# Kernel tuning notes

Hardware: AMD Instinct MI355X
Metric: run time of the kernel (lower is better)

The kernel has to match this reference:

```python
import jax, jax.numpy as jnp
import numpy as np

NUM_HEADS = 16
CAPACITY = 512
ROPE_BASE = 10000.0

def _rope_factor(positions, dim):
    # freqs = exp(linspace(0,-1,dim//2) * log(base)), shape (dim//2,)
    freqs = jnp.exp(jnp.linspace(0.0, -1.0, dim // 2) * jnp.log(jnp.float32(ROPE_BASE)))
    angles = positions[..., None] * freqs            # (..., seq, dim//2)
    return jnp.concatenate([jnp.sin(angles), jnp.cos(angles)], axis=-1)  # (..., seq, dim)

def setup_inputs() -> dict:
    key = jax.random.key(0)
    ks = jax.random.split(key, 6)
    B, Sq, Skv, D = 4, 4096, 4096, 1024
    return {
        "query_seq": jax.random.normal(ks[0], (B, Sq, D), jnp.float32),
        "value_seq": jax.random.normal(ks[1], (B, Skv, D), jnp.float32),
        "router_w": jax.random.normal(ks[2], (1, D), jnp.float32) * 0.02,
        "q_w": jax.random.normal(ks[3], (D, D), jnp.float32) * 0.02,
        "kv_w": jax.random.normal(ks[4], (2 * D, D), jnp.float32) * 0.02,
        "out_w": jax.random.normal(ks[5], (D, D), jnp.float32) * 0.02,
    }

def reference(query_seq, value_seq, router_w, q_w, kv_w, out_w):
    B, Sq, D = query_seq.shape
    Skv = value_seq.shape[1]
    H, C = NUM_HEADS, CAPACITY
    d = D // H

    # router + top-k capacity selection over the sequence dim
    rw = jnp.einsum("bsd,od->bs", query_seq, router_w).astype(jnp.float32)  # (B,Sq)
    top_w, top_idx = jax.lax.top_k(rw, C)                                   # (B,C)

    # gather selected queries
    resampled = jnp.take_along_axis(query_seq, top_idx[:, :, None], axis=1)  # (B,C,D)

    q = jnp.einsum("bcd,ed->bce", resampled, q_w)        # (B,C,H*d)
    kv = jnp.einsum("bsd,ed->bse", value_seq, kv_w)      # (B,Skv,2*H*d)
    k, v = jnp.split(kv, 2, axis=-1)

    q = q.reshape(B, C, H, d).transpose(0, 2, 1, 3)      # (B,H,C,d)
    k = k.reshape(B, Skv, H, d).transpose(0, 2, 1, 3)    # (B,H,Skv,d)
    v = v.reshape(B, Skv, H, d).transpose(0, 2, 1, 3)

    # RoPE-style elementwise modulation (faithful to source: x * cat(sin, cos))
    q_pos = top_idx.astype(jnp.float32)[:, None, :]      # (B,1,C)
    q = q * _rope_factor(q_pos, d)                       # (B,H,C,d)
    k_pos = jnp.arange(Skv, dtype=jnp.float32)[None, :]  # (1,Skv)
    k = k * _rope_factor(k_pos, d)[None]                 # broadcast over (B,H)

    # SDPA
    scores = jnp.einsum("bhcd,bhsd->bhcs", q, k) / jnp.sqrt(jnp.float32(d))
    att = jnp.einsum("bhcs,bhsd->bhcd", jax.nn.softmax(scores, axis=-1), v)

    att = att.transpose(0, 2, 1, 3).reshape(B, C, H * d)  # (B,C,D)
    att = jnp.einsum("bce,de->bcd", att, out_w)           # (B,C,D)

    # weighted scatter back to full sequence
    src = att * top_w[:, :, None]
    out = jnp.zeros_like(query_seq).at[jnp.arange(B)[:, None], top_idx].set(src)
    return out
```

## Files before the change

### kernel.cpp

```cpp
#include <hip/hip_runtime.h>
#include <hip/hip_bf16.h>

#define B_  4
#define SQ  4096
#define SKV 4096
#define DM  1024
#define NH  16
#define HD  64
#define CAP 512

#define ASPLIT 4
#define KVPER  (SKV / ASPLIT)
#define AITERS (KVPER / 64)

typedef __attribute__((ext_vector_type(8))) short    short8;
typedef __attribute__((ext_vector_type(8))) __bf16   bf16v8;
typedef __attribute__((ext_vector_type(4))) float    f32x4;
typedef __attribute__((ext_vector_type(4))) unsigned short ushort4v;

static __device__ __forceinline__ unsigned short f2bf(float f) {
    unsigned u = __float_as_uint(f);
    u += 0x7FFFu + ((u >> 16) & 1u);
    return (unsigned short)(u >> 16);
}

static __device__ __forceinline__ f32x4 mfma_bf16(short8 a, short8 b, f32x4 c) {
    return __builtin_amdgcn_mfma_f32_16x16x32_bf16(
        __builtin_bit_cast(bf16v8, a), __builtin_bit_cast(bf16v8, b), c, 0, 0, 0);
}

#define GLD16(gp, lp)                                                              \
    __builtin_amdgcn_global_load_lds(                                              \
        (__attribute__((address_space(1))) void*)(gp),                             \
        (__attribute__((address_space(3))) void*)(lp), 16, 0, 0)

__global__ void __launch_bounds__(256) k_convert(const float* __restrict__ in,
                                                 unsigned short* __restrict__ out) {
    size_t i = (size_t)blockIdx.x * 256 + threadIdx.x;
    float4 f = ((const float4*)in)[i];
    ushort4v o = { f2bf(f.x), f2bf(f.y), f2bf(f.z), f2bf(f.w) };
    ((ushort4v*)out)[i] = o;
}

__global__ void __launch_bounds__(256) k_rope(float* __restrict__ tab) {
    int g = blockIdx.x * 256 + threadIdx.x;
    int pos = g >> 6, i = g & 63, j = i & 31;
    float freq = expf(-(float)j * (logf(10000.0f) / 31.0f));
    float ang  = (float)pos * freq;
    tab[g] = (i < 32) ? sinf(ang) : cosf(ang);
}

__global__ void __launch_bounds__(256) k_router(const float* __restrict__ q,
                                                const float* __restrict__ wv,
                                                float* __restrict__ rw) {
    int row  = blockIdx.x * 4 + (threadIdx.x >> 6);
    int lane = threadIdx.x & 63;
    const float* p  = q  + (size_t)row * DM + lane * 16;
    const float* wp = wv + lane * 16;
    float s = 0.f;
#pragma unroll
    for (int j = 0; j < 4; j++) {
        float4 a = ((const float4*)p)[j];
        float4 b = ((const float4*)wp)[j];
        s += a.x * b.x + a.y * b.y + a.z * b.z + a.w * b.w;
    }
#pragma unroll
    for (int m = 32; m > 0; m >>= 1) s += __shfl_xor(s, m, 64);
    if (lane == 0) rw[row] = s;
}

__global__ void __launch_bounds__(1024) k_topk(const float* __restrict__ rw,
                                               int* __restrict__ sel,
                                               float* __restrict__ selw) {
    __shared__ unsigned long long keys[4096];
    int b = blockIdx.x, t = threadIdx.x;
    for (int i = t; i < 4096; i += 1024) {
        float v = rw[b * 4096 + i];
        unsigned u = __float_as_uint(v);
        u = (u & 0x80000000u) ? ~u : (u | 0x80000000u);
        keys[i] = ((unsigned long long)(~u) << 32) | (unsigned)i;
    }
    __syncthreads();
    for (int k = 2; k <= 4096; k <<= 1)
        for (int j = k >> 1; j > 0; j >>= 1) {
            for (int i = t; i < 4096; i += 1024) {
                int ixj = i ^ j;
                if (ixj > i) {
                    bool up = ((i & k) == 0);
                    unsigned long long a = keys[i], c = keys[ixj];
                    if ((a > c) == up) { keys[i] = c; keys[ixj] = a; }
                }
            }
            __syncthreads();
        }
    for (int i = t; i < 512; i += 1024) {
        unsigned idx = (unsigned)(keys[i] & 0xFFFFFFFFu);
        sel[b * 512 + i]  = (int)idx;
        selw[b * 512 + i] = rw[b * 4096 + idx];
    }
}

__global__ void __launch_bounds__(256) k_gather(const float* __restrict__ q,
                                                const int* __restrict__ sel,
                                                unsigned short* __restrict__ out) {
    int row = blockIdx.x;
    int b = row >> 9;
    int s = sel[row];
    const float4* src = (const float4*)(q + ((size_t)b * SQ + s) * DM);
    ushort4v* dst = (ushort4v*)(out + (size_t)row * DM);
    float4 f = src[threadIdx.x];
    ushort4v o = { f2bf(f.x), f2bf(f.y), f2bf(f.z), f2bf(f.w) };
    dst[threadIdx.x] = o;
}

template <int MODE, int BN>
__global__ void __launch_bounds__(256) k_gemm(
    const unsigned short* __restrict__ A,
    const unsigned short* __restrict__ Bw,
    int M, int N, int K,
    const float* __restrict__ rope_tab,
    const int* __restrict__ sel,
    const float* __restrict__ selw,
    unsigned short* __restrict__ ok,
    unsigned short* __restrict__ ov,
    unsigned short* __restrict__ obf,
    float* __restrict__ of) {
    constexpr int TN = BN / 32;
    __shared__ unsigned short lA[128 * 32];
    __shared__ unsigned short lB[BN * 32];
    const int tid = threadIdx.x;
    const int w = tid >> 6, lane = tid & 63, quad = lane >> 4, l16 = lane & 15;
    const int wr = w >> 1, wc = w & 1;
    const int mBase = blockIdx.y * 128, nBase = blockIdx.x * BN;

    f32x4 acc[4][TN] = {};

    for (int k0 = 0; k0 < K; k0 += 32) {
#pragma unroll
        for (int is = 0; is < 2; is++) {
            int slot = is * 256 + tid;
            int row = slot >> 2, sc = slot & 3;
            int kc = (sc - (row >> 1)) & 3;
            const char* ga = (const char*)A + (((size_t)(mBase + row) * K) + k0 + kc * 8) * 2;
            GLD16(ga, (char*)lA + slot * 16);
        }
#pragma unroll
        for (int is = 0; is < BN / 64; is++) {
            int slot = is * 256 + tid;
            int row = slot >> 2, sc = slot & 3;
            int kc = (sc - (row >> 1)) & 3;
            const char* gb = (const char*)Bw + (((size_t)(nBase + row) * K) + k0 + kc * 8) * 2;
            GLD16(gb, (char*)lB + slot * 16);
        }
        __syncthreads();
        short8 af[4], bfr[TN];
#pragma unroll
        for (int t = 0; t < 4; t++) {
            int r = wr * 64 + t * 16 + l16;
            af[t] = *(const short8*)&lA[r * 32 + (((quad + (r >> 1)) & 3) * 8)];
        }
#pragma unroll
        for (int t = 0; t < TN; t++) {
            int r = wc * (BN / 2) + t * 16 + l16;
            bfr[t] = *(const short8*)&lB[r * 32 + (((quad + (r >> 1)) & 3) * 8)];
        }
#pragma unroll
        for (int tm = 0; tm < 4; tm++)
#pragma unroll
            for (int tn = 0; tn < TN; tn++)
                acc[tm][tn] = mfma_bf16(af[tm], bfr[tn], acc[tm][tn]);
        __syncthreads();
    }

#pragma unroll
    for (int tm = 0; tm < 4; tm++) {
#pragma unroll
        for (int tn = 0; tn < TN; tn++) {
#pragma unroll
            for (int r = 0; r < 4; r++) {
                int m = mBase + wr * 64 + tm * 16 + quad * 4 + r;
                int n = nBase + wc * (BN / 2) + tn * 16 + l16;
                float v = acc[tm][tn][r];
                if constexpr (MODE == 0) {
                    int b = m >> 12, s = m & 4095;
                    if (n < 1024) {
                        int h = n >> 6, i = n & 63;
                        v *= rope_tab[(s << 6) | i];
                        ok[(((size_t)(b * NH + h) * SKV) + s) * HD + i] = f2bf(v);
                    } else {
                        int e = n - 1024, h = e >> 6, i = e & 63;
                        ov[(((size_t)(b * NH + h) * HD) + i) * SKV + s] = f2bf(v);
                    }
                } else if constexpr (MODE == 1) {
                    int b = m >> 9, c = m & 511;
                    int h = n >> 6, i = n & 63;
                    float rp = rope_tab[(sel[m] << 6) | i];
                    obf[(((size_t)(b * NH + h) * CAP) + c) * HD + i] =
                        f2bf(v * rp * 0.18033688011112042f);
                } else {
                    int b = m >> 9;
                    int s = sel[m];
                    of[(((size_t)b * SQ) + s) * DM + n] = v * selw[m];
                }
            }
        }
    }
}

__global__ void __launch_bounds__(256) k_attention(
    const unsigned short* __restrict__ Q,
    const unsigned short* __restrict__ Kg,
    const unsigned short* __restrict__ Vt,
    float* __restrict__ Opart,
    float* __restrict__ Lpart) {
    __shared__ unsigned short lK[64 * 72];
    __shared__ unsigned short lV[64 * 72];
    __shared__ unsigned short lP[4][32 * 72];
    const int bh = blockIdx.y, z = blockIdx.z;
    const int tid = threadIdx.x, w = tid >> 6, lane = tid & 63;
    const int quad = lane >> 4, l16 = lane & 15;
    const int qb = blockIdx.x * 128 + w * 32;
    const int base = z * KVPER;

    short8 qf[2][2];
#pragma unroll
    for (int rt = 0; rt < 2; rt++) {
        const unsigned short* qp = Q + ((size_t)bh * CAP + qb + rt * 16 + l16) * HD + quad * 8;
        qf[rt][0] = *(const short8*)qp;
        qf[rt][1] = *(const short8*)(qp + 32);
    }

    const unsigned short* kb = Kg + (size_t)bh * SKV * HD;
    const unsigned short* vb = Vt + (size_t)bh * HD * SKV;
    const int sr = tid >> 2, sp = tid & 3;

    f32x4 o[2][4] = {};
    f32x4 lsum[2] = {};
    short8 ones = (short8)0x3F80;

    short8 rk0, rk1, rv0, rv1;
    {
        const short8* srck = (const short8*)(kb + (size_t)(base + sr) * HD + sp * 16);
        rk0 = srck[0]; rk1 = srck[1];
        const short8* srcv = (const short8*)(vb + (size_t)sr * SKV + base + sp * 16);
        rv0 = srcv[0]; rv1 = srcv[1];
    }

    unsigned short* lPw = &lP[w][0];

    for (int it = 0; it < AITERS; it++) {
        __syncthreads();
        *(short8*)&lK[sr * 72 + sp * 16]     = rk0;
        *(short8*)&lK[sr * 72 + sp * 16 + 8] = rk1;
        *(short8*)&lV[sr * 72 + sp * 16]     = rv0;
        *(short8*)&lV[sr * 72 + sp * 16 + 8] = rv1;
        if (it + 1 < AITERS) {
            int s0 = base + (it + 1) * 64;
            const short8* srck = (const short8*)(kb + (size_t)(s0 + sr) * HD + sp * 16);
            rk0 = srck[0]; rk1 = srck[1];
            const short8* srcv = (const short8*)(vb + (size_t)sr * SKV + s0 + sp * 16);
            rv0 = srcv[0]; rv1 = srcv[1];
        }
        __syncthreads();

        f32x4 sc[2][4] = {};
#pragma unroll
        for (int tn = 0; tn < 4; tn++) {
            short8 kf0 = *(const short8*)&lK[(tn * 16 + l16) * 72 + quad * 8];
            short8 kf1 = *(const short8*)&lK[(tn * 16 + l16) * 72 + 32 + quad * 8];
#pragma unroll
            for (int rt = 0; rt < 2; rt++) {
                sc[rt][tn] = mfma_bf16(qf[rt][0], kf0, sc[rt][tn]);
                sc[rt][tn] = mfma_bf16(qf[rt][1], kf1, sc[rt][tn]);
            }
        }
#pragma unroll
        for (int rt = 0; rt < 2; rt++)
#pragma unroll
            for (int tn = 0; tn < 4; tn++)
#pragma unroll
                for (int r = 0; r < 4; r++)
                    lPw[(rt * 16 + quad * 4 + r) * 72 + tn * 16 + l16] =
                        f2bf(exp2f(fminf(sc[rt][tn][r], 86.f)));
#pragma unroll
        for (int kc = 0; kc < 2; kc++) {
            short8 pf0 = *(const short8*)&lPw[(l16) * 72 + kc * 32 + quad * 8];
            short8 pf1 = *(const short8*)&lPw[(16 + l16) * 72 + kc * 32 + quad * 8];
            lsum[0] = mfma_bf16(pf0, ones, lsum[0]);
            lsum[1] = mfma_bf16(pf1, ones, lsum[1]);
#pragma unroll
            for (int tn = 0; tn < 4; tn++) {
                short8 vf = *(const short8*)&lV[(tn * 16 + l16) * 72 + kc * 32 + quad * 8];
                o[0][tn] = mfma_bf16(pf0, vf, o[0][tn]);
                o[1][tn] = mfma_bf16(pf1, vf, o[1][tn]);
            }
        }
    }

    float* Ob = Opart + (((size_t)(z * 64 + bh)) * CAP + qb) * HD;
#pragma unroll
    for (int rt = 0; rt < 2; rt++)
#pragma unroll
        for (int tn = 0; tn < 4; tn++)
#pragma unroll
            for (int r = 0; r < 4; r++)
                Ob[(size_t)(rt * 16 + quad * 4 + r) * HD + tn * 16 + l16] = o[rt][tn][r];
    if (l16 == 0) {
#pragma unroll
        for (int rt = 0; rt < 2; rt++)
#pragma unroll
            for (int r = 0; r < 4; r++)
                Lpart[((size_t)(z * 64 + bh)) * CAP + qb + rt * 16 + quad * 4 + r] = lsum[rt][r];
    }
}

__global__ void __launch_bounds__(256) k_combine(
    const float* __restrict__ Opart, const float* __restrict__ Lpart,
    unsigned short* __restrict__ att) {
    int g = blockIdx.x * 256 + threadIdx.x;
    int dall = g & 1023, c = (g >> 10) & 511, b = g >> 19;
    int h = dall >> 6, dd = dall & 63;
    int bh = b * NH + h;
    float os = 0.f, ls = 0.f;
#pragma unroll
    for (int p = 0; p < ASPLIT; p++) {
        os += Opart[(((size_t)(p * 64 + bh)) * CAP + c) * HD + dd];
        ls += Lpart[((size_t)(p * 64 + bh)) * CAP + c];
    }
    att[g] = f2bf(os / ls);
}

extern "C" void kernel_launch(void* const* d_in, const int* in_sizes, int n_in,
                              void* d_out, int out_size, void* d_ws, size_t ws_size,
                              hipStream_t stream) {
    const float* query    = (const float*)d_in[0];
    const float* value    = (const float*)d_in[1];
    const float* router_w = (const float*)d_in[2];
    const float* q_w      = (const float*)d_in[3];
    const float* kv_w     = (const float*)d_in[4];
    const float* out_w    = (const float*)d_in[5];
    float* out = (float*)d_out;

    char* p = (char*)d_ws;
    unsigned short* value_bf = (unsigned short*)p; p += (size_t)B_ * SKV * DM * 2;
    unsigned short* kvw_bf   = (unsigned short*)p; p += (size_t)2 * DM * DM * 2;
    unsigned short* qw_bf    = (unsigned short*)p; p += (size_t)DM * DM * 2;
    unsigned short* ow_bf    = (unsigned short*)p; p += (size_t)DM * DM * 2;
    unsigned short* res_bf   = (unsigned short*)p; p += (size_t)B_ * CAP * DM * 2;
    unsigned short* q_attn   = (unsigned short*)p; p += (size_t)B_ * CAP * DM * 2;
    unsigned short* kbuf     = (unsigned short*)p; p += (size_t)B_ * SKV * DM * 2;
    unsigned short* vbuf     = (unsigned short*)p; p += (size_t)B_ * SKV * DM * 2;
    unsigned short* att_bf   = (unsigned short*)p; p += (size_t)B_ * CAP * DM * 2;
    float* rope_tab = (float*)p; p += (size_t)SKV * HD * 4;
    float* rw       = (float*)p; p += (size_t)B_ * SQ * 4;
    int*   sel      = (int*)p;   p += (size_t)B_ * CAP * 4;
    float* selw     = (float*)p; p += (size_t)B_ * CAP * 4;
    float* Opart = (float*)value_bf;
    float* Lpart = (float*)res_bf;

    hipMemsetAsync(d_out, 0, (size_t)out_size * sizeof(float), stream);

    k_convert<<<B_ * SKV * DM / 1024, 256, 0, stream>>>(value, value_bf);
    k_convert<<<2 * DM * DM / 1024, 256, 0, stream>>>(kv_w, kvw_bf);
    k_convert<<<DM * DM / 1024, 256, 0, stream>>>(q_w, qw_bf);
    k_convert<<<DM * DM / 1024, 256, 0, stream>>>(out_w, ow_bf);
    k_rope<<<SKV * HD / 256, 256, 0, stream>>>(rope_tab);
    k_router<<<B_ * SQ / 4, 256, 0, stream>>>(query, router_w, rw);
    k_topk<<<B_, 1024, 0, stream>>>(rw, sel, selw);
    k_gather<<<B_ * CAP, 256, 0, stream>>>(query, sel, res_bf);

    k_gemm<0, 128><<<dim3(2 * DM / 128, B_ * SKV / 128), 256, 0, stream>>>(
        value_bf, kvw_bf, B_ * SKV, 2 * DM, DM, rope_tab, nullptr, nullptr,
        kbuf, vbuf, nullptr, nullptr);
    k_gemm<1, 64><<<dim3(DM / 64, B_ * CAP / 128), 256, 0, stream>>>(
        res_bf, qw_bf, B_ * CAP, DM, DM, rope_tab, sel, nullptr,
        nullptr, nullptr, q_attn, nullptr);

    k_attention<<<dim3(CAP / 128, B_ * NH, ASPLIT), 256, 0, stream>>>(
        q_attn, kbuf, vbuf, Opart, Lpart);
    k_combine<<<B_ * CAP * DM / 256, 256, 0, stream>>>(Opart, Lpart, att_bf);

    k_gemm<2, 64><<<dim3(DM / 64, B_ * CAP / 128), 256, 0, stream>>>(
        att_bf, ow_bf, B_ * CAP, DM, DM, nullptr, sel, selw,
        nullptr, nullptr, nullptr, out);
}
```

Baseline: 523.7 us.

## Load attention K/V fragments straight to registers; swap MFMA operands for V-projection stores

The attention kernel no longer stages K and V tiles through shared memory behind two block barriers per iteration. Each wave now loads its K and V MFMA fragments directly from global memory into registers, with K double-buffered across iterations through a ping-pong loop. Separately, the KV projection GEMM swaps MFMA operands for the V half so the transposed V layout gets stores that are contiguous along the sequence dimension. The cost is that each wave issues redundant global (cache-hit) loads instead of sharing tiles, and register pressure goes up.

```diff
diff --git a/kernel.cpp b/kernel.cpp
--- a/kernel.cpp
+++ b/kernel.cpp
@@ -1,5 +1,6 @@
 #include <hip/hip_runtime.h>
 #include <hip/hip_bf16.h>
+#include <type_traits>
 
 #define B_  4
 #define SQ  4096
@@ -131,79 +132,96 @@
     const int tid = threadIdx.x;
     const int w = tid >> 6, lane = tid & 63, quad = lane >> 4, l16 = lane & 15;
     const int wr = w >> 1, wc = w & 1;
-    const int mBase = blockIdx.y * 128, nBase = blockIdx.x * BN;
-
-    f32x4 acc[4][TN] = {};
-
-    for (int k0 = 0; k0 < K; k0 += 32) {
-#pragma unroll
-        for (int is = 0; is < 2; is++) {
-            int slot = is * 256 + tid;
-            int row = slot >> 2, sc = slot & 3;
-            int kc = (sc - (row >> 1)) & 3;
-            const char* ga = (const char*)A + (((size_t)(mBase + row) * K) + k0 + kc * 8) * 2;
-            GLD16(ga, (char*)lA + slot * 16);
+    const int mBase = blockIdx.y * 128;
+    const int nBase = blockIdx.x * BN;
+
+    auto run = [&](auto swap_tag) {
+        constexpr bool SWAP = decltype(swap_tag)::value;
+        f32x4 acc[4][TN] = {};
+        for (int k0 = 0; k0 < K; k0 += 32) {
+#pragma unroll
+            for (int is = 0; is < 2; is++) {
+                int slot = is * 256 + tid;
+                int row = slot >> 2, sc = slot & 3;
+                int kc = (sc - (row >> 1)) & 3;
+                const char* ga = (const char*)A + (((size_t)(mBase + row) * K) + k0 + kc * 8) * 2;
+                GLD16(ga, (char*)lA + slot * 16);
+            }
+#pragma unroll
+            for (int is = 0; is < BN / 64; is++) {
+                int slot = is * 256 + tid;
+                int row = slot >> 2, sc = slot & 3;
+                int kc = (sc - (row >> 1)) & 3;
+                const char* gb = (const char*)Bw + (((size_t)(nBase + row) * K) + k0 + kc * 8) * 2;
+                GLD16(gb, (char*)lB + slot * 16);
+            }
+            __syncthreads();
+            short8 af[4], bfr[TN];
+#pragma unroll
+            for (int t = 0; t < 4; t++) {
+                int r = wr * 64 + t * 16 + l16;
+                af[t] = *(const short8*)&lA[r * 32 + (((quad + (r >> 1)) & 3) * 8)];
+            }
+#pragma unroll
+            for (int t = 0; t < TN; t++) {
+                int r = wc * (BN / 2) + t * 16 + l16;
+                bfr[t] = *(const short8*)&lB[r * 32 + (((quad + (r >> 1)) & 3) * 8)];
+            }
+#pragma unroll
+            for (int tm = 0; tm < 4; tm++)
+#pragma unroll
+                for (int tn = 0; tn < TN; tn++) {
+                    if constexpr (SWAP)
+                        acc[tm][tn] = mfma_bf16(bfr[tn], af[tm], acc[tm][tn]);
+                    else
+                        acc[tm][tn] = mfma_bf16(af[tm], bfr[tn], acc[tm][tn]);
+                }
+            __syncthreads();
         }
-#pragma unroll
-        for (int is = 0; is < BN / 64; is++) {
-            int slot = is * 256 + tid;
-            int row = slot >> 2, sc = slot & 3;
-            int kc = (sc - (row >> 1)) & 3;
-            const char* gb = (const char*)Bw + (((size_t)(nBase + row) * K) + k0 + kc * 8) * 2;
-            GLD16(gb, (char*)lB + slot * 16);
+
+#pragma unroll
+        for (int tm = 0; tm < 4; tm++) {
+#pragma unroll
+            for (int tn = 0; tn < TN; tn++) {
+#pragma unroll
+                for (int r = 0; r < 4; r++) {
+                    float v = acc[tm][tn][r];
+                    if constexpr (SWAP) {
+                        int n = nBase + wc * (BN / 2) + tn * 16 + quad * 4 + r;
+                        int m = mBase + wr * 64 + tm * 16 + l16;
+                        int e = n - 1024, h = e >> 6, i = e & 63;
+                        int b = m >> 12, s = m & 4095;
+                        ov[(((size_t)(b * NH + h) * HD) + i) * SKV + s] = f2bf(v);
+                    } else {
+                        int m = mBase + wr * 64 + tm * 16 + quad * 4 + r;
+                        int n = nBase + wc * (BN / 2) + tn * 16 + l16;
+                        if constexpr (MODE == 4) {
+                            int b = m >> 12, s = m & 4095;
+                            int h = n >> 6, i = n & 63;
+                            v *= rope_tab[(s << 6) | i];
+                            ok[(((size_t)(b * NH + h) * SKV) + s) * HD + i] = f2bf(v);
+                        } else if constexpr (MODE == 1) {
+                            int b = m >> 9, c = m & 511;
+                            int h = n >> 6, i = n & 63;
+                            float rp = rope_tab[(sel[m] << 6) | i];
+                            obf[(((size_t)(b * NH + h) * CAP) + c) * HD + i] =
+                                f2bf(v * rp * 0.18033688011112042f);
+                        } else {
+                            int b = m >> 9;
+                            int s = sel[m];
+                            of[(((size_t)b * SQ) + s) * DM + n] = v * selw[m];
+                        }
+                    }
+                }
+            }
         }
-        __syncthreads();
-        short8 af[4], bfr[TN];
-#pragma unroll
-        for (int t = 0; t < 4; t++) {
-            int r = wr * 64 + t * 16 + l16;
-            af[t] = *(const short8*)&lA[r * 32 + (((quad + (r >> 1)) & 3) * 8)];
-        }
-#pragma unroll
-        for (int t = 0; t < TN; t++) {
-            int r = wc * (BN / 2) + t * 16 + l16;
-            bfr[t] = *(const short8*)&lB[r * 32 + (((quad + (r >> 1)) & 3) * 8)];
-        }
-#pragma unroll
-        for (int tm = 0; tm < 4; tm++)
-#pragma unroll
-            for (int tn = 0; tn < TN; tn++)
-                acc[tm][tn] = mfma_bf16(af[tm], bfr[tn], acc[tm][tn]);
-        __syncthreads();
-    }
-
-#pragma unroll
-    for (int tm = 0; tm < 4; tm++) {
-#pragma unroll
-        for (int tn = 0; tn < TN; tn++) {
-#pragma unroll
-            for (int r = 0; r < 4; r++) {
-                int m = mBase + wr * 64 + tm * 16 + quad * 4 + r;
-                int n = nBase + wc * (BN / 2) + tn * 16 + l16;
-                float v = acc[tm][tn][r];
-                if constexpr (MODE == 0) {
-                    int b = m >> 12, s = m & 4095;
-                    if (n < 1024) {
-                        int h = n >> 6, i = n & 63;
-                        v *= rope_tab[(s << 6) | i];
-                        ok[(((size_t)(b * NH + h) * SKV) + s) * HD + i] = f2bf(v);
-                    } else {
-                        int e = n - 1024, h = e >> 6, i = e & 63;
-                        ov[(((size_t)(b * NH + h) * HD) + i) * SKV + s] = f2bf(v);
-                    }
-                } else if constexpr (MODE == 1) {
-                    int b = m >> 9, c = m & 511;
-                    int h = n >> 6, i = n & 63;
-                    float rp = rope_tab[(sel[m] << 6) | i];
-                    obf[(((size_t)(b * NH + h) * CAP) + c) * HD + i] =
-                        f2bf(v * rp * 0.18033688011112042f);
-                } else {
-                    int b = m >> 9;
-                    int s = sel[m];
-                    of[(((size_t)b * SQ) + s) * DM + n] = v * selw[m];
-                }
-            }
-        }
+    };
+
+    if constexpr (MODE == 4) {
+        if (nBase < 1024) run(std::false_type{});
+        else              run(std::true_type{});
+    } else {
+        run(std::false_type{});
     }
 }
 
@@ -213,8 +231,6 @@
     const unsigned short* __restrict__ Vt,
     float* __restrict__ Opart,
     float* __restrict__ Lpart) {
-    __shared__ unsigned short lK[64 * 72];
-    __shared__ unsigned short lV[64 * 72];
     __shared__ unsigned short lP[4][32 * 72];
     const int bh = blockIdx.y, z = blockIdx.z;
     const int tid = threadIdx.x, w = tid >> 6, lane = tid & 63;
@@ -230,49 +246,43 @@
         qf[rt][1] = *(const short8*)(qp + 32);
     }
 
-    const unsigned short* kb = Kg + (size_t)bh * SKV * HD;
-    const unsigned short* vb = Vt + (size_t)bh * HD * SKV;
-    const int sr = tid >> 2, sp = tid & 3;
+    const unsigned short* kp = Kg + (size_t)bh * SKV * HD + (size_t)(base + l16) * HD + quad * 8;
+    const unsigned short* vp = Vt + (size_t)bh * HD * SKV + (size_t)l16 * SKV + base + quad * 8;
 
     f32x4 o[2][4] = {};
     f32x4 lsum[2] = {};
     short8 ones = (short8)0x3F80;
-
-    short8 rk0, rk1, rv0, rv1;
-    {
-        const short8* srck = (const short8*)(kb + (size_t)(base + sr) * HD + sp * 16);
-        rk0 = srck[0]; rk1 = srck[1];
-        const short8* srcv = (const short8*)(vb + (size_t)sr * SKV + base + sp * 16);
-        rv0 = srcv[0]; rv1 = srcv[1];
-    }
-
     unsigned short* lPw = &lP[w][0];
 
-    for (int it = 0; it < AITERS; it++) {
-        __syncthreads();
-        *(short8*)&lK[sr * 72 + sp * 16]     = rk0;
-        *(short8*)&lK[sr * 72 + sp * 16 + 8] = rk1;
-        *(short8*)&lV[sr * 72 + sp * 16]     = rv0;
-        *(short8*)&lV[sr * 72 + sp * 16 + 8] = rv1;
+    short8 kfA[4][2], kfB[4][2], vf[4][2];
+#pragma unroll
+    for (int tn = 0; tn < 4; tn++)
+#pragma unroll
+        for (int kc = 0; kc < 2; kc++)
+            kfA[tn][kc] = *(const short8*)(kp + (size_t)(tn * 16) * HD + kc * 32);
+
+    auto body = [&](int it, short8 (&kc_cur)[4][2], short8 (&kc_nxt)[4][2]) {
+        const int soff = it * 64;
+#pragma unroll
+        for (int tn = 0; tn < 4; tn++)
+#pragma unroll
+            for (int kc = 0; kc < 2; kc++)
+                vf[tn][kc] = *(const short8*)(vp + (size_t)(tn * 16) * SKV + soff + kc * 32);
+        f32x4 sc[2][4] = {};
+#pragma unroll
+        for (int tn = 0; tn < 4; tn++)
+#pragma unroll
+            for (int rt = 0; rt < 2; rt++) {
+                sc[rt][tn] = mfma_bf16(qf[rt][0], kc_cur[tn][0], sc[rt][tn]);
+                sc[rt][tn] = mfma_bf16(qf[rt][1], kc_cur[tn][1], sc[rt][tn]);
+            }
         if (it + 1 < AITERS) {
-            int s0 = base + (it + 1) * 64;
-            const short8* srck = (const short8*)(kb + (size_t)(s0 + sr) * HD + sp * 16);
-            rk0 = srck[0]; rk1 = srck[1];
-            const short8* srcv = (const short8*)(vb + (size_t)sr * SKV + s0 + sp * 16);
-            rv0 = srcv[0]; rv1 = srcv[1];
-        }
-        __syncthreads();
-
-        f32x4 sc[2][4] = {};
-#pragma unroll
-        for (int tn = 0; tn < 4; tn++) {
-            short8 kf0 = *(const short8*)&lK[(tn * 16 + l16) * 72 + quad * 8];
-            short8 kf1 = *(const short8*)&lK[(tn * 16 + l16) * 72 + 32 + quad * 8];
-#pragma unroll
-            for (int rt = 0; rt < 2; rt++) {
-                sc[rt][tn] = mfma_bf16(qf[rt][0], kf0, sc[rt][tn]);
-                sc[rt][tn] = mfma_bf16(qf[rt][1], kf1, sc[rt][tn]);
-            }
+#pragma unroll
+            for (int tn = 0; tn < 4; tn++)
+#pragma unroll
+                for (int kc = 0; kc < 2; kc++)
+                    kc_nxt[tn][kc] =
+                        *(const short8*)(kp + (size_t)(soff + 64 + tn * 16) * HD + kc * 32);
         }
 #pragma unroll
         for (int rt = 0; rt < 2; rt++)
@@ -290,11 +300,15 @@
             lsum[1] = mfma_bf16(pf1, ones, lsum[1]);
 #pragma unroll
             for (int tn = 0; tn < 4; tn++) {
-                short8 vf = *(const short8*)&lV[(tn * 16 + l16) * 72 + kc * 32 + quad * 8];
-                o[0][tn] = mfma_bf16(pf0, vf, o[0][tn]);
-                o[1][tn] = mfma_bf16(pf1, vf, o[1][tn]);
+                o[0][tn] = mfma_bf16(pf0, vf[tn][kc], o[0][tn]);
+                o[1][tn] = mfma_bf16(pf1, vf[tn][kc], o[1][tn]);
             }
         }
+    };
+
+    for (int it = 0; it < AITERS; it += 2) {
+        body(it, kfA, kfB);
+        body(it + 1, kfB, kfA);
     }
 
     float* Ob = Opart + (((size_t)(z * 64 + bh)) * CAP + qb) * HD;
@@ -369,7 +383,7 @@
     k_topk<<<B_, 1024, 0, stream>>>(rw, sel, selw);
     k_gather<<<B_ * CAP, 256, 0, stream>>>(query, sel, res_bf);
 
-    k_gemm<0, 128><<<dim3(2 * DM / 128, B_ * SKV / 128), 256, 0, stream>>>(
+    k_gemm<4, 128><<<dim3(2 * DM / 128, B_ * SKV / 128), 256, 0, stream>>>(
         value_bf, kvw_bf, B_ * SKV, 2 * DM, DM, rope_tab, nullptr, nullptr,
         kbuf, vbuf, nullptr, nullptr);
     k_gemm<1, 64><<<dim3(DM / 64, B_ * CAP / 128), 256, 0, stream>>>(
```

New measurement: 526.6 us. About the same (+0.6%).
